# Kernel optimization log

Hardware: AMD Instinct MI355X
Metric: run time of the kernel (lower is better)

## Reference

```python
import jax, jax.numpy as jnp
import numpy as np


def setup_inputs() -> dict:
    key0 = jax.random.key(0)
    ks = jax.random.split(key0, 6)
    b, q, k = 4, 256, 1024
    emb_q = emb_k = emb_v = 256
    h = 128
    query = jax.random.normal(ks[0], (b, q, emb_q), dtype=jnp.float32)
    key = jax.random.normal(ks[1], (b, k, emb_k), dtype=jnp.float32)
    value = jax.random.normal(ks[2], (b, k, emb_v), dtype=jnp.float32)
    # linear_uniform_ style init: U(-1/sqrt(in), 1/sqrt(in))
    wq = jax.random.uniform(ks[3], (emb_q, h), minval=-1.0, maxval=1.0) / np.sqrt(emb_q)
    wk = jax.random.uniform(ks[4], (emb_k, h), minval=-1.0, maxval=1.0) / np.sqrt(emb_k)
    wv = jax.random.uniform(ks[5], (h,), minval=-1.0, maxval=1.0) / np.sqrt(h)
    return {"query": query, "key": key, "value": value,
            "weight_query": wq.astype(jnp.float32),
            "weight_key": wk.astype(jnp.float32),
            "weight_value": wv.astype(jnp.float32)}


def reference(query, key, value, weight_query, weight_key, weight_value):
    # Additive (Bahdanau) attention.
    Hq = jnp.einsum('bqe,eh->bqh', query, weight_query)   # (b, q, h)
    Hk = jnp.einsum('bke,eh->bkh', key, weight_key)       # (b, k, h)
    # broadcast-add + tanh: (b, q, k, h)
    H = jnp.tanh(Hq[:, :, None, :] + Hk[:, None, :, :])
    z = jnp.einsum('bqkh,h->bqk', H, weight_value)        # scores (b, q, k)
    a = jax.nn.softmax(z, axis=-1)                        # (b, q, k)
    out = jnp.einsum('bqk,bkv->bqv', a, value)            # (b, q, emb_v)
    return out, a
```

## Files before the change

kernel.cpp:

```cpp
#include <hip/hip_runtime.h>


#define L2E 1.4426950408889634f

__global__ __launch_bounds__(256) void aa_proj_kernel(
    const float* __restrict__ query, const float* __restrict__ key,
    const float* __restrict__ wq, const float* __restrict__ wk,
    float* __restrict__ Eq, float* __restrict__ Ek)
{
    __shared__ float rows_s[16 * 256];
    const int i = blockIdx.x;
    const int t = threadIdx.x;

    const float* src;
    const float* W;
    float* dst;
    if (i < 64) {
        const int r0 = i * 16;
        src = query + r0 * 256; W = wq; dst = Eq + r0 * 128;
    } else {
        const int r0 = (i - 64) * 16;
        src = key + r0 * 256; W = wk; dst = Ek + r0 * 128;
    }

#pragma unroll
    for (int j = 0; j < 4; ++j) {
        const int f = t * 4 + j * 1024;
        *(float4*)&rows_s[f] = *(const float4*)&src[f];
    }
    __syncthreads();

    const int rgr = t >> 5;
    const int hg = t & 31;
    const int ri0 = rgr * 2;
    const int h0 = hg * 4;

    float acc0[4] = {0.f, 0.f, 0.f, 0.f};
    float acc1[4] = {0.f, 0.f, 0.f, 0.f};

    for (int e = 0; e < 256; e += 4) {
        float a0[4], a1[4];
        *(float4*)a0 = *(const float4*)&rows_s[ri0 * 256 + e];
        *(float4*)a1 = *(const float4*)&rows_s[(ri0 + 1) * 256 + e];
#pragma unroll
        for (int j = 0; j < 4; ++j) {
            float w[4];
            *(float4*)w = *(const float4*)&W[(e + j) * 128 + h0];
#pragma unroll
            for (int c = 0; c < 4; ++c) {
                acc0[c] = fmaf(a0[j], w[c], acc0[c]);
                acc1[c] = fmaf(a1[j], w[c], acc1[c]);
            }
        }
    }

    float o0[4], o1[4];
#pragma unroll
    for (int c = 0; c < 4; ++c) {
        o0[c] = __builtin_amdgcn_exp2f(acc0[c] * (2.0f * L2E));
        o1[c] = __builtin_amdgcn_exp2f(acc1[c] * (2.0f * L2E));
    }
    *(float4*)&dst[ri0 * 128 + h0] = *(float4*)o0;
    *(float4*)&dst[(ri0 + 1) * 128 + h0] = *(float4*)o1;
}

__global__ __launch_bounds__(256) void aa_score_kernel(
    const float* __restrict__ Eq, const float* __restrict__ Ek,
    const float* __restrict__ wv, float* __restrict__ z)
{
    __shared__ float eq_s[16 * 128];
    __shared__ float ek_s[64 * 132];
    __shared__ float wv_s[128];

    const int bid = blockIdx.x;
    const int b = bid >> 8;
    const int qt = (bid >> 4) & 15;
    const int kt = bid & 15;
    const int q0g = b * 256 + qt * 16;
    const int k0g = b * 1024 + kt * 64;
    const int t = threadIdx.x;

    const float* eqsrc = Eq + q0g * 128;
#pragma unroll
    for (int j = 0; j < 2; ++j) {
        const int f = t * 4 + j * 1024;
        *(float4*)&eq_s[f] = *(const float4*)&eqsrc[f];
    }
    const float* eksrc = Ek + k0g * 128;
#pragma unroll
    for (int j = 0; j < 8; ++j) {
        const int f = t * 4 + j * 1024;
        const int ki = f >> 7;
        const int h = f & 127;
        *(float4*)&ek_s[ki * 132 + h] = *(const float4*)&eksrc[f];
    }
    if (t < 128) wv_s[t] = wv[t];
    __syncthreads();

    float wsum = 0.f;
#pragma unroll
    for (int j = 0; j < 32; ++j) {
        float w4[4];
        *(float4*)w4 = *(const float4*)&wv_s[j * 4];
        wsum += (w4[0] + w4[1]) + (w4[2] + w4[3]);
    }

    const int qp = t >> 5;
    const int kp = t & 31;
    const float* eqa = eq_s + (qp * 2) * 128;
    const float* eqb = eqa + 128;
    const float* eka = ek_s + kp * 132;
    const float* ekb = eka + 32 * 132;

    float acc00 = 0.f, acc01 = 0.f, acc10 = 0.f, acc11 = 0.f;

#pragma unroll 4
    for (int h = 0; h < 128; h += 4) {
        float a0[4], a1[4], b0[4], b1[4], w[4];
        *(float4*)a0 = *(const float4*)(eqa + h);
        *(float4*)a1 = *(const float4*)(eqb + h);
        *(float4*)b0 = *(const float4*)(eka + h);
        *(float4*)b1 = *(const float4*)(ekb + h);
        *(float4*)w  = *(const float4*)(wv_s + h);
#pragma unroll
        for (int j = 0; j < 4; ++j) {
            const float r00 = __builtin_amdgcn_rcpf(fmaf(a0[j], b0[j], 1.0f));
            const float r01 = __builtin_amdgcn_rcpf(fmaf(a0[j], b1[j], 1.0f));
            const float r10 = __builtin_amdgcn_rcpf(fmaf(a1[j], b0[j], 1.0f));
            const float r11 = __builtin_amdgcn_rcpf(fmaf(a1[j], b1[j], 1.0f));
            acc00 = fmaf(w[j], r00, acc00);
            acc01 = fmaf(w[j], r01, acc01);
            acc10 = fmaf(w[j], r10, acc10);
            acc11 = fmaf(w[j], r11, acc11);
        }
    }

    const int kl = kt * 64 + kp;
    float* zr0 = z + (size_t)(q0g + qp * 2) * 1024 + kl;
    float* zr1 = zr0 + 1024;
    zr0[0]  = fmaf(-2.f, acc00, wsum);
    zr0[32] = fmaf(-2.f, acc01, wsum);
    zr1[0]  = fmaf(-2.f, acc10, wsum);
    zr1[32] = fmaf(-2.f, acc11, wsum);
}

__global__ __launch_bounds__(256) void aa_softmax_kernel(
    const float* __restrict__ z, float* __restrict__ a)
{
    const int row = blockIdx.x;
    const int t = threadIdx.x;
    const float* zr = z + (size_t)row * 1024;

    float x[4];
    *(float4*)x = *(const float4*)&zr[t * 4];

    float m = fmaxf(fmaxf(x[0], x[1]), fmaxf(x[2], x[3]));
#pragma unroll
    for (int off = 32; off; off >>= 1) m = fmaxf(m, __shfl_xor(m, off));

    __shared__ float redm[4];
    __shared__ float reds[4];
    const int wid = t >> 6;
    if ((t & 63) == 0) redm[wid] = m;
    __syncthreads();
    m = fmaxf(fmaxf(redm[0], redm[1]), fmaxf(redm[2], redm[3]));

    float e[4];
    float s = 0.f;
#pragma unroll
    for (int j = 0; j < 4; ++j) {
        e[j] = __builtin_amdgcn_exp2f((x[j] - m) * L2E);
        s += e[j];
    }
#pragma unroll
    for (int off = 32; off; off >>= 1) s += __shfl_xor(s, off);
    if ((t & 63) == 0) reds[wid] = s;
    __syncthreads();
    s = reds[0] + reds[1] + reds[2] + reds[3];

    const float inv = __builtin_amdgcn_rcpf(s);
    float o[4];
#pragma unroll
    for (int j = 0; j < 4; ++j) o[j] = e[j] * inv;
    *(float4*)&a[(size_t)row * 1024 + t * 4] = *(float4*)o;
}

__global__ __launch_bounds__(256) void aa_pv_partial_kernel(
    const float* __restrict__ a, const float* __restrict__ value,
    float* __restrict__ part)
{
    __shared__ float a_s[8][128];
    __shared__ float red_s[4][2048];
    const int bid = blockIdx.x;
    const int b  = bid >> 8;
    const int qt = (bid >> 3) & 31;
    const int kt = bid & 7;
    const int t = threadIdx.x;

    {
        const int qs = t >> 5;
        const int k0 = (t & 31) * 4;
        const float* arow = a + (size_t)(b * 256 + qt * 8 + qs) * 1024 + kt * 128;
        *(float4*)&a_s[qs][k0] = *(const float4*)&arow[k0];
    }
    __syncthreads();

    const int w = t >> 6;
    const int lane = t & 63;
    const int v0 = lane * 4;
    const float* vp = value + (size_t)b * 262144
                    + (size_t)(kt * 128 + w * 32) * 256 + v0;

    float acc[8][4] = {};

#pragma unroll
    for (int k4 = 0; k4 < 8; ++k4) {
        float vv[4][4];
#pragma unroll
        for (int r = 0; r < 4; ++r)
            *(float4*)vv[r] = *(const float4*)(vp + (size_t)(k4 * 4 + r) * 256);
        float aq[8][4];
#pragma unroll
        for (int q = 0; q < 8; ++q)
            *(float4*)aq[q] = *(const float4*)&a_s[q][w * 32 + k4 * 4];
#pragma unroll
        for (int q = 0; q < 8; ++q)
#pragma unroll
            for (int r = 0; r < 4; ++r)
#pragma unroll
                for (int c = 0; c < 4; ++c)
                    acc[q][c] = fmaf(aq[q][r], vv[r][c], acc[q][c]);
    }

    float* rs = &red_s[w][v0];
#pragma unroll
    for (int q = 0; q < 8; ++q)
        *(float4*)(rs + q * 256) = *(float4*)acc[q];
    __syncthreads();

    const int e0 = t * 8;
    float s[8];
#pragma unroll
    for (int c = 0; c < 8; ++c) s[c] = red_s[0][e0 + c];
#pragma unroll
    for (int ww = 1; ww < 4; ++ww)
#pragma unroll
        for (int c = 0; c < 8; ++c) s[c] += red_s[ww][e0 + c];

    float* po = part + (size_t)bid * 2048 + e0;
    *(float4*)(po)     = *(float4*)&s[0];
    *(float4*)(po + 4) = *(float4*)&s[4];
}

__global__ __launch_bounds__(256) void aa_pv_reduce_kernel(
    const float* __restrict__ part, float* __restrict__ out)
{
    const int idx = blockIdx.x * 256 + threadIdx.x;
    const int o = idx * 4;
    const int row = o >> 8;
    const int v = o & 255;
    const int b = row >> 8;
    const int q = row & 255;
    const int qt = q >> 3;
    const int qr = q & 7;
    const float* p = part + (size_t)((b * 32 + qt) * 8) * 2048 + qr * 256 + v;

    float s[4] = {0.f, 0.f, 0.f, 0.f};
#pragma unroll
    for (int kt = 0; kt < 8; ++kt) {
        float x[4];
        *(float4*)x = *(const float4*)(p + (size_t)kt * 2048);
        s[0] += x[0]; s[1] += x[1]; s[2] += x[2]; s[3] += x[3];
    }
    *(float4*)&out[o] = *(float4*)s;
}

extern "C" void kernel_launch(void* const* d_in, const int* in_sizes, int n_in,
                              void* d_out, int out_size, void* d_ws, size_t ws_size,
                              hipStream_t stream)
{
    const float* query = (const float*)d_in[0];
    const float* key   = (const float*)d_in[1];
    const float* value = (const float*)d_in[2];
    const float* wq    = (const float*)d_in[3];
    const float* wk    = (const float*)d_in[4];
    const float* wv    = (const float*)d_in[5];

    float* out   = (float*)d_out;
    float* a_out = out + 4 * 256 * 256;

    float* ws = (float*)d_ws;
    float* Eq   = ws;
    float* Ek   = ws + 131072;
    float* z    = ws + 131072 + 524288;
    float* part = ws + 131072 + 524288 + 1048576;

    aa_proj_kernel<<<320, 256, 0, stream>>>(query, key, wq, wk, Eq, Ek);
    aa_score_kernel<<<1024, 256, 0, stream>>>(Eq, Ek, wv, z);
    aa_softmax_kernel<<<1024, 256, 0, stream>>>(z, a_out);
    aa_pv_partial_kernel<<<1024, 256, 0, stream>>>(a_out, value, part);
    aa_pv_reduce_kernel<<<256, 256, 0, stream>>>(part, out);
}
```

Before: 59.34 us.

## Batch reciprocals in score loop, stage weights in LDS, widen PV query tile

The score kernel now combines four 1/(1+x·y) terms over a common denominator, so each group of four h values uses one reciprocal instead of four. This trades transcendental-unit work for extra multiplies and adds some risk of overflow or precision loss in the products. The projection kernel stages weight chunks in shared memory instead of reading them from global memory per thread. The PV partial kernel handles 16 query rows per block instead of 8, which halves the grid and reuses each value load across more rows, at the cost of more registers and larger partial buffers.

```diff
diff --git a/kernel.cpp b/kernel.cpp
--- a/kernel.cpp
+++ b/kernel.cpp
@@ -9,6 +9,7 @@
     float* __restrict__ Eq, float* __restrict__ Ek)
 {
     __shared__ float rows_s[16 * 256];
+    __shared__ float w_s[64 * 128];
     const int i = blockIdx.x;
     const int t = threadIdx.x;
 
@@ -28,7 +29,6 @@
         const int f = t * 4 + j * 1024;
         *(float4*)&rows_s[f] = *(const float4*)&src[f];
     }
-    __syncthreads();
 
     const int rgr = t >> 5;
     const int hg = t & 31;
@@ -38,18 +38,28 @@
     float acc0[4] = {0.f, 0.f, 0.f, 0.f};
     float acc1[4] = {0.f, 0.f, 0.f, 0.f};
 
-    for (int e = 0; e < 256; e += 4) {
-        float a0[4], a1[4];
-        *(float4*)a0 = *(const float4*)&rows_s[ri0 * 256 + e];
-        *(float4*)a1 = *(const float4*)&rows_s[(ri0 + 1) * 256 + e];
-#pragma unroll
-        for (int j = 0; j < 4; ++j) {
-            float w[4];
-            *(float4*)w = *(const float4*)&W[(e + j) * 128 + h0];
-#pragma unroll
-            for (int c = 0; c < 4; ++c) {
-                acc0[c] = fmaf(a0[j], w[c], acc0[c]);
-                acc1[c] = fmaf(a1[j], w[c], acc1[c]);
+    for (int ec = 0; ec < 256; ec += 64) {
+        __syncthreads();
+#pragma unroll
+        for (int j = 0; j < 8; ++j) {
+            const int f = t * 4 + j * 1024;
+            *(float4*)&w_s[f] = *(const float4*)&W[ec * 128 + f];
+        }
+        __syncthreads();
+
+        for (int e = 0; e < 64; e += 4) {
+            float a0[4], a1[4];
+            *(float4*)a0 = *(const float4*)&rows_s[ri0 * 256 + ec + e];
+            *(float4*)a1 = *(const float4*)&rows_s[(ri0 + 1) * 256 + ec + e];
+#pragma unroll
+            for (int j = 0; j < 4; ++j) {
+                float w[4];
+                *(float4*)w = *(const float4*)&w_s[(e + j) * 128 + h0];
+#pragma unroll
+                for (int c = 0; c < 4; ++c) {
+                    acc0[c] = fmaf(a0[j], w[c], acc0[c]);
+                    acc1[c] = fmaf(a1[j], w[c], acc1[c]);
+                }
             }
         }
     }
@@ -113,6 +123,19 @@
     const float* ekb = eka + 32 * 132;
 
     float acc00 = 0.f, acc01 = 0.f, acc10 = 0.f, acc11 = 0.f;
+
+    auto quad = [](const float* x, const float* y, const float* w, float& acc) {
+        const float A = fmaf(x[0], y[0], 1.0f);
+        const float B = fmaf(x[1], y[1], 1.0f);
+        const float C = fmaf(x[2], y[2], 1.0f);
+        const float D = fmaf(x[3], y[3], 1.0f);
+        const float AB = A * B;
+        const float CD = C * D;
+        const float n01 = fmaf(w[1], A, w[0] * B);
+        const float n23 = fmaf(w[3], C, w[2] * D);
+        const float num = fmaf(n01, CD, n23 * AB);
+        acc = fmaf(num, __builtin_amdgcn_rcpf(AB * CD), acc);
+    };
 
 #pragma unroll 4
     for (int h = 0; h < 128; h += 4) {
@@ -122,17 +145,10 @@
         *(float4*)b0 = *(const float4*)(eka + h);
         *(float4*)b1 = *(const float4*)(ekb + h);
         *(float4*)w  = *(const float4*)(wv_s + h);
-#pragma unroll
-        for (int j = 0; j < 4; ++j) {
-            const float r00 = __builtin_amdgcn_rcpf(fmaf(a0[j], b0[j], 1.0f));
-            const float r01 = __builtin_amdgcn_rcpf(fmaf(a0[j], b1[j], 1.0f));
-            const float r10 = __builtin_amdgcn_rcpf(fmaf(a1[j], b0[j], 1.0f));
-            const float r11 = __builtin_amdgcn_rcpf(fmaf(a1[j], b1[j], 1.0f));
-            acc00 = fmaf(w[j], r00, acc00);
-            acc01 = fmaf(w[j], r01, acc01);
-            acc10 = fmaf(w[j], r10, acc10);
-            acc11 = fmaf(w[j], r11, acc11);
-        }
+        quad(a0, b0, w, acc00);
+        quad(a0, b1, w, acc01);
+        quad(a1, b0, w, acc10);
+        quad(a1, b1, w, acc11);
     }
 
     const int kl = kt * 64 + kp;
@@ -189,18 +205,20 @@
     const float* __restrict__ a, const float* __restrict__ value,
     float* __restrict__ part)
 {
-    __shared__ float a_s[8][128];
-    __shared__ float red_s[4][2048];
+    __shared__ float a_s[16][128];
+    __shared__ float red_s[4][4096];
     const int bid = blockIdx.x;
-    const int b  = bid >> 8;
-    const int qt = (bid >> 3) & 31;
+    const int b  = bid >> 7;
+    const int qt = (bid >> 3) & 15;
     const int kt = bid & 7;
     const int t = threadIdx.x;
 
-    {
-        const int qs = t >> 5;
-        const int k0 = (t & 31) * 4;
-        const float* arow = a + (size_t)(b * 256 + qt * 8 + qs) * 1024 + kt * 128;
+#pragma unroll
+    for (int j = 0; j < 2; ++j) {
+        const int f = t * 4 + j * 1024;
+        const int qs = f >> 7;
+        const int k0 = f & 127;
+        const float* arow = a + (size_t)(b * 256 + qt * 16 + qs) * 1024 + kt * 128;
         *(float4*)&a_s[qs][k0] = *(const float4*)&arow[k0];
     }
     __syncthreads();
@@ -211,45 +229,48 @@
     const float* vp = value + (size_t)b * 262144
                     + (size_t)(kt * 128 + w * 32) * 256 + v0;
 
-    float acc[8][4] = {};
-
-#pragma unroll
+    float acc[16][4] = {};
+
+#pragma unroll 2
     for (int k4 = 0; k4 < 8; ++k4) {
         float vv[4][4];
 #pragma unroll
         for (int r = 0; r < 4; ++r)
             *(float4*)vv[r] = *(const float4*)(vp + (size_t)(k4 * 4 + r) * 256);
-        float aq[8][4];
-#pragma unroll
-        for (int q = 0; q < 8; ++q)
-            *(float4*)aq[q] = *(const float4*)&a_s[q][w * 32 + k4 * 4];
-#pragma unroll
-        for (int q = 0; q < 8; ++q)
+#pragma unroll
+        for (int q = 0; q < 16; ++q) {
+            float aq[4];
+            *(float4*)aq = *(const float4*)&a_s[q][w * 32 + k4 * 4];
 #pragma unroll
             for (int r = 0; r < 4; ++r)
 #pragma unroll
                 for (int c = 0; c < 4; ++c)
-                    acc[q][c] = fmaf(aq[q][r], vv[r][c], acc[q][c]);
+                    acc[q][c] = fmaf(aq[r], vv[r][c], acc[q][c]);
+        }
     }
 
     float* rs = &red_s[w][v0];
 #pragma unroll
-    for (int q = 0; q < 8; ++q)
+    for (int q = 0; q < 16; ++q)
         *(float4*)(rs + q * 256) = *(float4*)acc[q];
     __syncthreads();
 
-    const int e0 = t * 8;
-    float s[8];
-#pragma unroll
-    for (int c = 0; c < 8; ++c) s[c] = red_s[0][e0 + c];
-#pragma unroll
-    for (int ww = 1; ww < 4; ++ww)
-#pragma unroll
-        for (int c = 0; c < 8; ++c) s[c] += red_s[ww][e0 + c];
-
-    float* po = part + (size_t)bid * 2048 + e0;
-    *(float4*)(po)     = *(float4*)&s[0];
-    *(float4*)(po + 4) = *(float4*)&s[4];
+    const int g = t >> 6;
+    const int l4 = (t & 63) * 4;
+    float* po = part + (size_t)bid * 4096;
+#pragma unroll
+    for (int c = 0; c < 4; ++c) {
+        const int i = g * 1024 + c * 256 + l4;
+        float s[4];
+        *(float4*)s = *(const float4*)&red_s[0][i];
+#pragma unroll
+        for (int ww = 1; ww < 4; ++ww) {
+            float x[4];
+            *(float4*)x = *(const float4*)&red_s[ww][i];
+            s[0] += x[0]; s[1] += x[1]; s[2] += x[2]; s[3] += x[3];
+        }
+        *(float4*)(po + i) = *(float4*)s;
+    }
 }
 
 __global__ __launch_bounds__(256) void aa_pv_reduce_kernel(
@@ -261,15 +282,15 @@
     const int v = o & 255;
     const int b = row >> 8;
     const int q = row & 255;
-    const int qt = q >> 3;
-    const int qr = q & 7;
-    const float* p = part + (size_t)((b * 32 + qt) * 8) * 2048 + qr * 256 + v;
+    const int qt = q >> 4;
+    const int qr = q & 15;
+    const float* p = part + (size_t)((b * 16 + qt) * 8) * 4096 + qr * 256 + v;
 
     float s[4] = {0.f, 0.f, 0.f, 0.f};
 #pragma unroll
     for (int kt = 0; kt < 8; ++kt) {
         float x[4];
-        *(float4*)x = *(const float4*)(p + (size_t)kt * 2048);
+        *(float4*)x = *(const float4*)(p + (size_t)kt * 4096);
         s[0] += x[0]; s[1] += x[1]; s[2] += x[2]; s[3] += x[3];
     }
     *(float4*)&out[o] = *(float4*)s;
@@ -298,6 +319,6 @@
     aa_proj_kernel<<<320, 256, 0, stream>>>(query, key, wq, wk, Eq, Ek);
     aa_score_kernel<<<1024, 256, 0, stream>>>(Eq, Ek, wv, z);
     aa_softmax_kernel<<<1024, 256, 0, stream>>>(z, a_out);
-    aa_pv_partial_kernel<<<1024, 256, 0, stream>>>(a_out, value, part);
+    aa_pv_partial_kernel<<<512, 256, 0, stream>>>(a_out, value, part);
     aa_pv_reduce_kernel<<<256, 256, 0, stream>>>(part, out);
 }
```

Result: faster. 53.47 us (-9.9%).
